# Kernel optimization log

Measured on AMD Instinct MI355X. Metric: run time of the kernel, lower is better.

The kernel has to match this reference:

```python
import jax, jax.numpy as jnp
import numpy as np

N_NODES = 50000
N_EDGES = 1600000
D_IN = 128
D_OUT = 128


def setup_inputs() -> dict:
    key = jax.random.key(0)
    ks = jax.random.split(key, 8)
    feat = jax.random.normal(ks[0], (N_NODES, D_IN), dtype=jnp.float32)
    src = jax.random.randint(ks[1], (N_EDGES,), 0, N_NODES, dtype=jnp.int32)
    dst = jax.random.randint(ks[2], (N_EDGES,), 0, N_NODES, dtype=jnp.int32)
    # Xavier-uniform-ish init for the two linear layers
    lim = float(np.sqrt(6.0 / (D_IN + D_OUT))) * float(np.sqrt(2.0))  # gain=relu
    W_self = jax.random.uniform(ks[3], (D_OUT, D_IN), jnp.float32, -lim, lim)
    b_self = jnp.zeros((D_OUT,), jnp.float32)
    W_neigh = jax.random.uniform(ks[4], (D_OUT, D_IN), jnp.float32, -lim, lim)
    b_neigh = jnp.zeros((D_OUT,), jnp.float32)
    return {
        "feat": feat, "src": src, "dst": dst,
        "W_self": W_self, "b_self": b_self,
        "W_neigh": W_neigh, "b_neigh": b_neigh,
    }


def reference(feat, src, dst, W_self, b_self, W_neigh, b_neigh):
    """GraphSAGE 'mean' aggregator, eval mode (feat_drop=0).

    in_feats == out_feats -> lin_before_mp is False:
      h_neigh = fc_neigh(mean_{u in N(v)} feat[u])
      rst     = fc_self(feat[v]) + h_neigh
    Zero in-degree nodes get a zero neighbor vector (DGL mean semantics).
    """
    n = feat.shape[0]
    msg = feat[src]                                            # [E, D_in] gather
    agg = jax.ops.segment_sum(msg, dst, num_segments=n)        # [N, D_in] scatter-add
    deg = jax.ops.segment_sum(jnp.ones_like(src, feat.dtype), dst, num_segments=n)
    h_neigh = agg / jnp.maximum(deg, 1.0)[:, None]             # segment mean
    h_neigh = h_neigh @ W_neigh.T + b_neigh                    # fc_neigh
    h_self = feat @ W_self.T + b_self                          # fc_self
    return h_self + h_neigh
```

## Files before the change

### kernel.cpp

```cpp
#include <hip/hip_runtime.h>
#include <hip/hip_fp16.h>

#define D 128
#define BLOCK 256
#define CAP 128
#define BINSH 7
#define MAXBINS 392
#define BCAP 6144
#define CHUNK 2048

typedef __attribute__((ext_vector_type(2))) float floatx2;
typedef __attribute__((ext_vector_type(4))) float floatx4;
typedef __attribute__((ext_vector_type(8))) _Float16 half8;

union U4H8 { uint4 u; half8 h; };

__global__ __launch_bounds__(256) void sage_prep(
    const float4* __restrict__ feat4, unsigned int* __restrict__ feat8, int n4,
    int ncvt_blocks,
    const float* __restrict__ W_self, const float* __restrict__ W_neigh,
    const float* __restrict__ b_self, const float* __restrict__ b_neigh,
    unsigned int* __restrict__ wcat2, float* __restrict__ biascat,
    int* __restrict__ bin_cursor)
{
    int b = blockIdx.x, t = threadIdx.x;
    if (b < ncvt_blocks) {
        int i = b * 256 + t;
        if (i < n4) {
            float4 f = feat4[i];
            unsigned int r = __builtin_amdgcn_cvt_pk_fp8_f32(f.x, f.y, 0u, false);
            r = __builtin_amdgcn_cvt_pk_fp8_f32(f.z, f.w, r, true);
            feat8[i] = r;
        }
    } else if (b < ncvt_blocks + 64) {
        int idx = (b - ncvt_blocks) * 256 + t;
        int n = idx >> 7;
        int k = (idx & 127) * 2;
        float a, bb;
        if (k < 128) { a = W_self[n * 128 + k];        bb = W_self[n * 128 + k + 1]; }
        else         { a = W_neigh[n * 128 + k - 128]; bb = W_neigh[n * 128 + k - 127]; }
        __half2 h = __floats2half2_rn(a, bb);
        wcat2[idx] = *reinterpret_cast<unsigned int*>(&h);
        if (idx < 128) biascat[idx] = b_self[idx] + b_neigh[idx];
    } else {
        for (int i = t; i < MAXBINS; i += 256) bin_cursor[i] = 0;
    }
}

__global__ __launch_bounds__(256) void sage_bin(
    const int* __restrict__ src, const int* __restrict__ dst,
    int* __restrict__ bin_cursor, unsigned int* __restrict__ bins, int n_edges)
{
    __shared__ int hist[MAXBINS];
    __shared__ int base[MAXBINS];
    int t = threadIdx.x;
    if (t < MAXBINS - 256) hist[256 + t] = 0;
    hist[t] = 0;
    __syncthreads();

    int e0 = blockIdx.x * CHUNK;
    unsigned int item[8];
    int binr[8];
    #pragma unroll
    for (int k = 0; k < 8; ++k) {
        int i = e0 + k * 256 + t;
        if (i < n_edges) {
            int d = dst[i];
            int s = src[i];
            int bin = d >> BINSH;
            int r = atomicAdd(&hist[bin], 1);
            item[k] = ((unsigned int)(d & 127) << 16) | (unsigned int)s;
            binr[k] = (bin << 16) | r;
        } else binr[k] = -1;
    }
    __syncthreads();
    #pragma unroll
    for (int bb = 0; bb < 2; ++bb) {
        int bin = t + bb * 256;
        if (bin < MAXBINS) {
            int h = hist[bin];
            base[bin] = h ? atomicAdd(&bin_cursor[bin], h) : 0;
        }
    }
    __syncthreads();
    #pragma unroll
    for (int k = 0; k < 8; ++k) {
        if (binr[k] >= 0) {
            int bin = binr[k] >> 16;
            int pos = base[bin] + (binr[k] & 0xFFFF);
            if (pos < BCAP)
                bins[(size_t)bin * BCAP + pos] = item[k];
        }
    }
}

__global__ __launch_bounds__(256) void sage_bucket(
    const unsigned int* __restrict__ bins, const int* __restrict__ bin_cursor,
    unsigned short* __restrict__ bucket, int* __restrict__ cnt_g, int n_nodes)
{
    __shared__ int cnt[128];
    __shared__ unsigned short buck[128 * CAP];
    int b = blockIdx.x;
    int t = threadIdx.x;
    if (t < 128) cnt[t] = 0;
    __syncthreads();

    int n_items = min(bin_cursor[b], BCAP);
    const unsigned int* bp = bins + (size_t)b * BCAP;
    for (int i = t; i < n_items; i += 256) {
        unsigned int it = bp[i];
        int d = it >> 16;
        int c = atomicAdd(&cnt[d], 1);
        if (c < CAP) buck[d * CAP + c] = (unsigned short)(it & 0xFFFFu);
    }
    __syncthreads();

    const uint4* lb = (const uint4*)buck;
    uint4* gb = (uint4*)(bucket + (size_t)b * 128 * CAP);
    #pragma unroll
    for (int k = 0; k < 8; ++k)
        gb[k * 256 + t] = lb[k * 256 + t];
    if (t < 128) {
        int node = b * 128 + t;
        if (node < n_nodes) cnt_g[node] = cnt[t];
    }
}

__device__ inline void addq(float* acc, unsigned int q) {
    floatx2 lo = __builtin_amdgcn_cvt_pk_f32_fp8(q, false);
    floatx2 hi = __builtin_amdgcn_cvt_pk_f32_fp8(q, true);
    acc[0] += lo[0]; acc[1] += lo[1]; acc[2] += hi[0]; acc[3] += hi[1];
}

__device__ inline void add16(float* acc, uint4 r) {
    addq(acc + 0,  r.x);
    addq(acc + 4,  r.y);
    addq(acc + 8,  r.z);
    addq(acc + 12, r.w);
}

__global__ __launch_bounds__(BLOCK) void sage_agg_gemm(
    const float* __restrict__ feat,
    const uint4* __restrict__ feat84,
    const int* __restrict__ cnt_g,
    const unsigned short* __restrict__ bucket,
    const uint4* __restrict__ wcat4,
    const float* __restrict__ biascat,
    float* __restrict__ out, int n_nodes)
{
    __shared__ _Float16 mean_lds[16][136];

    int v0 = blockIdx.x * 16;
    int t = threadIdx.x;
    int wave = t >> 6;
    int lane = t & 63;

    {
        int g = (lane >> 4) & 3;
        int eo = (lane >> 3) & 1;
        int h = lane & 7;
        int lo = 2 * g + eo;

        for (int v = wave; v < 16; v += 4) {
            int node = v0 + v;
            if (node >= n_nodes) break;
            int deg = cnt_g[node];
            int cv = min(deg, CAP);
            const unsigned short* b = bucket + (size_t)node * CAP;

            float acc[16];
            #pragma unroll
            for (int i = 0; i < 16; ++i) acc[i] = 0.0f;

            int e = 0;
            for (; e + 32 <= cv; e += 32) {
                int s0 = b[e + lo];
                int s1 = b[e + 8 + lo];
                int s2 = b[e + 16 + lo];
                int s3 = b[e + 24 + lo];
                uint4 r0 = feat84[(size_t)s0 * 8 + h];
                uint4 r1 = feat84[(size_t)s1 * 8 + h];
                uint4 r2 = feat84[(size_t)s2 * 8 + h];
                uint4 r3 = feat84[(size_t)s3 * 8 + h];
                add16(acc, r0); add16(acc, r1); add16(acc, r2); add16(acc, r3);
            }
            #pragma unroll
            for (int k = 0; k < 4; ++k) {
                int idx = e + 8 * k + lo;
                if (idx < cv) {
                    uint4 r = feat84[(size_t)b[idx] * 8 + h];
                    add16(acc, r);
                }
            }

            #pragma unroll
            for (int i = 0; i < 16; ++i) {
                acc[i] += __shfl_xor(acc[i], 8);
                acc[i] += __shfl_xor(acc[i], 16);
                acc[i] += __shfl_xor(acc[i], 32);
            }
            if (lane < 8) {
                float inv = 1.0f / fmaxf((float)deg, 1.0f);
                unsigned int p[8];
                #pragma unroll
                for (int i = 0; i < 8; ++i) {
                    __half2 hh = __floats2half2_rn(acc[2 * i] * inv, acc[2 * i + 1] * inv);
                    p[i] = *reinterpret_cast<unsigned int*>(&hh);
                }
                uint4 lo4 = { p[0], p[1], p[2], p[3] };
                uint4 hi4 = { p[4], p[5], p[6], p[7] };
                uint4* xp = (uint4*)&mean_lds[v][h * 16];
                xp[0] = lo4;
                xp[1] = hi4;
            }
        }
    }
    __syncthreads();

    {
        int m16 = lane & 15;
        int kq = lane >> 4;
        int m = v0 + m16;
        int msafe = (m < n_nodes) ? m : 0;

        half8 a[8];
        const float4* fp = (const float4*)(feat + (size_t)msafe * D);
        #pragma unroll
        for (int kt = 0; kt < 4; ++kt) {
            float4 f0 = fp[kt * 8 + kq * 2];
            float4 f1 = fp[kt * 8 + kq * 2 + 1];
            half8 hh;
            hh[0] = (_Float16)f0.x; hh[1] = (_Float16)f0.y;
            hh[2] = (_Float16)f0.z; hh[3] = (_Float16)f0.w;
            hh[4] = (_Float16)f1.x; hh[5] = (_Float16)f1.y;
            hh[6] = (_Float16)f1.z; hh[7] = (_Float16)f1.w;
            a[kt] = hh;
        }
        const uint4* mrow = (const uint4*)&mean_lds[m16][0];
        #pragma unroll
        for (int kt = 0; kt < 4; ++kt) {
            U4H8 u; u.u = mrow[kt * 4 + kq];
            a[4 + kt] = u.h;
        }

        #pragma unroll
        for (int cc = 0; cc < 2; ++cc) {
            int ct = wave * 2 + cc;
            floatx4 acc = { 0.f, 0.f, 0.f, 0.f };
            #pragma unroll
            for (int kt = 0; kt < 8; ++kt) {
                U4H8 w; w.u = wcat4[(size_t)(ct * 16 + m16) * 32 + kt * 4 + kq];
                acc = __builtin_amdgcn_mfma_f32_16x16x32_f16(a[kt], w.h, acc, 0, 0, 0);
            }
            float bias = biascat[ct * 16 + m16];
            #pragma unroll
            for (int i = 0; i < 4; ++i) {
                int r = v0 + kq * 4 + i;
                if (r < n_nodes)
                    out[(size_t)r * D + ct * 16 + m16] = acc[i] + bias;
            }
        }
    }
}

extern "C" void kernel_launch(void* const* d_in, const int* in_sizes, int n_in,
                              void* d_out, int out_size, void* d_ws, size_t ws_size,
                              hipStream_t stream)
{
    const float* feat    = (const float*)d_in[0];
    const int*   src     = (const int*)d_in[1];
    const int*   dst     = (const int*)d_in[2];
    const float* W_self  = (const float*)d_in[3];
    const float* b_self  = (const float*)d_in[4];
    const float* W_neigh = (const float*)d_in[5];
    const float* b_neigh = (const float*)d_in[6];
    float* out = (float*)d_out;

    int n_nodes = in_sizes[0] / D;
    int n_edges = in_sizes[1];
    int nbins = (n_nodes + 127) >> 7;

    unsigned short* bucket = (unsigned short*)d_ws;
    int* cnt_g = (int*)(bucket + (size_t)nbins * 128 * CAP);
    unsigned int* feat8 = (unsigned int*)(cnt_g + n_nodes);
    unsigned int* wcat = feat8 + (size_t)n_nodes * (D / 4);
    float* biascat = (float*)(wcat + 128 * 128);
    int* bin_cursor = (int*)(biascat + 128);

    unsigned int* bins = (unsigned int*)d_out;

    int n4 = n_nodes * (D / 4);
    int ncvt = (n4 + 255) / 256;
    sage_prep<<<ncvt + 64 + 1, 256, 0, stream>>>(
        (const float4*)feat, feat8, n4, ncvt,
        W_self, W_neigh, b_self, b_neigh, wcat, biascat, bin_cursor);
    sage_bin<<<(n_edges + CHUNK - 1) / CHUNK, 256, 0, stream>>>(
        src, dst, bin_cursor, bins, n_edges);
    sage_bucket<<<nbins, 256, 0, stream>>>(
        bins, bin_cursor, bucket, cnt_g, n_nodes);
    sage_agg_gemm<<<(n_nodes + 15) / 16, BLOCK, 0, stream>>>(
        feat, (const uint4*)feat8, cnt_g, bucket,
        (const uint4*)wcat, biascat, out, n_nodes);
}
```

Measured before the change: 209.9 us.

## Replace two-pass binned bucketing with direct global-atomic scatter into per-node buckets

Drops the two-stage bucketing (block-local histogram into coarse bins, then a per-bin LDS bucket pass) and replaces it with one kernel that does a global atomicAdd on each destination node's counter and writes the source id straight into that node's bucket slot. This removes a kernel launch and the intermediate bins buffer round trip. In exchange it issues 1.6M global atomics to random addresses and scattered 2-byte writes, which may contend or be slower than the LDS-staged approach. The neighbour order within a bucket also becomes nondeterministic.

```diff
diff --git a/kernel.cpp b/kernel.cpp
--- a/kernel.cpp
+++ b/kernel.cpp
@@ -4,10 +4,6 @@
 #define D 128
 #define BLOCK 256
 #define CAP 128
-#define BINSH 7
-#define MAXBINS 392
-#define BCAP 6144
-#define CHUNK 2048
 
 typedef __attribute__((ext_vector_type(2))) float floatx2;
 typedef __attribute__((ext_vector_type(4))) float floatx4;
@@ -21,7 +17,7 @@
     const float* __restrict__ W_self, const float* __restrict__ W_neigh,
     const float* __restrict__ b_self, const float* __restrict__ b_neigh,
     unsigned int* __restrict__ wcat2, float* __restrict__ biascat,
-    int* __restrict__ bin_cursor)
+    int* __restrict__ cnt_g, int n_nodes)
 {
     int b = blockIdx.x, t = threadIdx.x;
     if (b < ncvt_blocks) {
@@ -43,86 +39,32 @@
         wcat2[idx] = *reinterpret_cast<unsigned int*>(&h);
         if (idx < 128) biascat[idx] = b_self[idx] + b_neigh[idx];
     } else {
-        for (int i = t; i < MAXBINS; i += 256) bin_cursor[i] = 0;
-    }
-}
-
-__global__ __launch_bounds__(256) void sage_bin(
+        int base = (b - ncvt_blocks - 64) * 256 + t;
+        for (int i = base; i < n_nodes; i += 8 * 256) cnt_g[i] = 0;
+    }
+}
+
+__global__ __launch_bounds__(256) void sage_scatter(
     const int* __restrict__ src, const int* __restrict__ dst,
-    int* __restrict__ bin_cursor, unsigned int* __restrict__ bins, int n_edges)
-{
-    __shared__ int hist[MAXBINS];
-    __shared__ int base[MAXBINS];
-    int t = threadIdx.x;
-    if (t < MAXBINS - 256) hist[256 + t] = 0;
-    hist[t] = 0;
-    __syncthreads();
-
-    int e0 = blockIdx.x * CHUNK;
-    unsigned int item[8];
-    int binr[8];
-    #pragma unroll
-    for (int k = 0; k < 8; ++k) {
-        int i = e0 + k * 256 + t;
-        if (i < n_edges) {
-            int d = dst[i];
-            int s = src[i];
-            int bin = d >> BINSH;
-            int r = atomicAdd(&hist[bin], 1);
-            item[k] = ((unsigned int)(d & 127) << 16) | (unsigned int)s;
-            binr[k] = (bin << 16) | r;
-        } else binr[k] = -1;
-    }
-    __syncthreads();
-    #pragma unroll
-    for (int bb = 0; bb < 2; ++bb) {
-        int bin = t + bb * 256;
-        if (bin < MAXBINS) {
-            int h = hist[bin];
-            base[bin] = h ? atomicAdd(&bin_cursor[bin], h) : 0;
-        }
-    }
-    __syncthreads();
-    #pragma unroll
-    for (int k = 0; k < 8; ++k) {
-        if (binr[k] >= 0) {
-            int bin = binr[k] >> 16;
-            int pos = base[bin] + (binr[k] & 0xFFFF);
-            if (pos < BCAP)
-                bins[(size_t)bin * BCAP + pos] = item[k];
-        }
-    }
-}
-
-__global__ __launch_bounds__(256) void sage_bucket(
-    const unsigned int* __restrict__ bins, const int* __restrict__ bin_cursor,
-    unsigned short* __restrict__ bucket, int* __restrict__ cnt_g, int n_nodes)
-{
-    __shared__ int cnt[128];
-    __shared__ unsigned short buck[128 * CAP];
-    int b = blockIdx.x;
-    int t = threadIdx.x;
-    if (t < 128) cnt[t] = 0;
-    __syncthreads();
-
-    int n_items = min(bin_cursor[b], BCAP);
-    const unsigned int* bp = bins + (size_t)b * BCAP;
-    for (int i = t; i < n_items; i += 256) {
-        unsigned int it = bp[i];
-        int d = it >> 16;
-        int c = atomicAdd(&cnt[d], 1);
-        if (c < CAP) buck[d * CAP + c] = (unsigned short)(it & 0xFFFFu);
-    }
-    __syncthreads();
-
-    const uint4* lb = (const uint4*)buck;
-    uint4* gb = (uint4*)(bucket + (size_t)b * 128 * CAP);
-    #pragma unroll
-    for (int k = 0; k < 8; ++k)
-        gb[k * 256 + t] = lb[k * 256 + t];
-    if (t < 128) {
-        int node = b * 128 + t;
-        if (node < n_nodes) cnt_g[node] = cnt[t];
+    int* __restrict__ cnt_g, unsigned short* __restrict__ bucket, int n_edges)
+{
+    int i0 = (blockIdx.x * 256 + (int)threadIdx.x) * 4;
+    if (i0 + 3 < n_edges) {
+        int4 s4 = *(const int4*)(src + i0);
+        int4 d4 = *(const int4*)(dst + i0);
+        int s[4] = { s4.x, s4.y, s4.z, s4.w };
+        int d[4] = { d4.x, d4.y, d4.z, d4.w };
+        #pragma unroll
+        for (int k = 0; k < 4; ++k) {
+            int c = atomicAdd(&cnt_g[d[k]], 1);
+            if (c < CAP) bucket[(size_t)d[k] * CAP + c] = (unsigned short)s[k];
+        }
+    } else {
+        for (int i = i0; i < n_edges; ++i) {
+            int dd = dst[i];
+            int c = atomicAdd(&cnt_g[dd], 1);
+            if (c < CAP) bucket[(size_t)dd * CAP + c] = (unsigned short)src[i];
+        }
     }
 }
 
@@ -278,26 +220,20 @@
 
     int n_nodes = in_sizes[0] / D;
     int n_edges = in_sizes[1];
-    int nbins = (n_nodes + 127) >> 7;
 
     unsigned short* bucket = (unsigned short*)d_ws;
-    int* cnt_g = (int*)(bucket + (size_t)nbins * 128 * CAP);
+    int* cnt_g = (int*)(bucket + (size_t)n_nodes * CAP);
     unsigned int* feat8 = (unsigned int*)(cnt_g + n_nodes);
     unsigned int* wcat = feat8 + (size_t)n_nodes * (D / 4);
     float* biascat = (float*)(wcat + 128 * 128);
-    int* bin_cursor = (int*)(biascat + 128);
-
-    unsigned int* bins = (unsigned int*)d_out;
 
     int n4 = n_nodes * (D / 4);
     int ncvt = (n4 + 255) / 256;
-    sage_prep<<<ncvt + 64 + 1, 256, 0, stream>>>(
+    sage_prep<<<ncvt + 64 + 8, 256, 0, stream>>>(
         (const float4*)feat, feat8, n4, ncvt,
-        W_self, W_neigh, b_self, b_neigh, wcat, biascat, bin_cursor);
-    sage_bin<<<(n_edges + CHUNK - 1) / CHUNK, 256, 0, stream>>>(
-        src, dst, bin_cursor, bins, n_edges);
-    sage_bucket<<<nbins, 256, 0, stream>>>(
-        bins, bin_cursor, bucket, cnt_g, n_nodes);
+        W_self, W_neigh, b_self, b_neigh, wcat, biascat, cnt_g, n_nodes);
+    sage_scatter<<<(n_edges + 1023) / 1024, 256, 0, stream>>>(
+        src, dst, cnt_g, bucket, n_edges);
     sage_agg_gemm<<<(n_nodes + 15) / 16, BLOCK, 0, stream>>>(
         feat, (const uint4*)feat8, cnt_g, bucket,
         (const uint4*)wcat, biascat, out, n_nodes);
```

After: 283.0 us. 34.9% more time.
